# Kernel tuning notes

Hardware: AMD Instinct MI355X
Metric: run time of the kernel (lower is better)

## Reference

```python
import jax, jax.numpy as jnp
import numpy as np

N_NODES = 100000
N_EDGES = 3200000
IN_DIM = 64
HID = 64


def setup_inputs() -> dict:
    key = jax.random.key(0)
    ks = jax.random.split(key, 12)
    x = jax.random.normal(ks[0], (N_NODES, IN_DIM), dtype=jnp.float32)
    edge_index = jax.random.randint(ks[1], (2, N_EDGES), 0, N_NODES, dtype=jnp.int64)
    tau = jax.random.uniform(ks[2], (N_NODES, 1), dtype=jnp.float32)
    d1 = IN_DIM + 1  # augmented feature dim
    s1 = 1.0 / np.sqrt(d1)
    s2 = 1.0 / np.sqrt(HID)
    # SAGEConv: out = lin_l(mean_aggr) + lin_r(x); bias lives in lin_l. Weights stored [in, out].
    W1l = jax.random.uniform(ks[3], (d1, HID), jnp.float32, -s1, s1)
    b1l = jax.random.uniform(ks[4], (HID,), jnp.float32, -s1, s1)
    W1r = jax.random.uniform(ks[5], (d1, HID), jnp.float32, -s1, s1)
    W2l = jax.random.uniform(ks[6], (HID, HID), jnp.float32, -s2, s2)
    b2l = jax.random.uniform(ks[7], (HID,), jnp.float32, -s2, s2)
    W2r = jax.random.uniform(ks[8], (HID, HID), jnp.float32, -s2, s2)
    Wfc = jax.random.uniform(ks[9], (HID, 1), jnp.float32, -s2, s2)
    bfc = jax.random.uniform(ks[10], (1,), jnp.float32, -s2, s2)
    return {"x": x, "edge_index": edge_index, "tau": tau,
            "W1l": W1l, "b1l": b1l, "W1r": W1r,
            "W2l": W2l, "b2l": b2l, "W2r": W2r,
            "Wfc": Wfc, "bfc": bfc}


def _sage_conv(x, src, dst, Wl, bl, Wr, n_nodes):
    # mean aggregation of source-node features onto target nodes
    summed = jax.ops.segment_sum(x[src], dst, num_segments=n_nodes)  # [N, d]
    deg = jax.ops.segment_sum(jnp.ones(src.shape[0], x.dtype), dst, num_segments=n_nodes)
    mean = summed / jnp.maximum(deg, 1.0)[:, None]
    return mean @ Wl + bl + x @ Wr


def reference(x, edge_index, tau, W1l, b1l, W1r, W2l, b2l, W2r, Wfc, bfc):
    src, dst = edge_index[0], edge_index[1]
    n = x.shape[0]
    h = jnp.concatenate([x, tau], axis=1)  # augment_features: append tau column
    h = jax.nn.relu(_sage_conv(h, src, dst, W1l, b1l, W1r, n))
    h = jax.nn.relu(_sage_conv(h, src, dst, W2l, b2l, W2r, n))
    return h @ Wfc + bfc  # [N, 1]
```

## Files before the change

kernel.cpp:

```cpp
#include <hip/hip_runtime.h>
#include <hip/hip_bf16.h>
#include <hip/hip_fp16.h>
#include <hip/hip_fp8.h>


#define BSH 7
#define NBKT 782
#define NBLK 512
#define PER 6250
#define CAPH 3072
#define AB2 256

typedef _Float16 half8 __attribute__((ext_vector_type(8)));
typedef float floatx4 __attribute__((ext_vector_type(4)));
typedef float floatx2 __attribute__((ext_vector_type(2)));

struct h4s { __half2 lo, hi; };

#if __has_builtin(__builtin_amdgcn_cvt_pk_f32_fp8)
template <bool HI>
__device__ __forceinline__ float2 f8x2_to_f2(int v) {
    floatx2 r = __builtin_amdgcn_cvt_pk_f32_fp8(v, HI);
    return make_float2(r.x, r.y);
}
#else
template <bool HI>
__device__ __forceinline__ float2 f8x2_to_f2(int v) {
    unsigned short u = HI ? (unsigned short)(((unsigned)v) >> 16)
                          : (unsigned short)(v & 0xFFFF);
    __half2_raw r = __hip_cvt_fp8x2_to_halfraw2((__hip_fp8x2_storage_t)u, __HIP_E4M3);
    return __half22float2(*(__half2*)&r);
}
#endif

#if __has_builtin(__builtin_amdgcn_cvt_pk_fp8_f32)
__device__ __forceinline__ unsigned f4_to_f8x4(float a, float b, float c, float d) {
    int lo = __builtin_amdgcn_cvt_pk_fp8_f32(a, b, 0, false);
    return (unsigned)__builtin_amdgcn_cvt_pk_fp8_f32(c, d, lo, true);
}
__device__ __forceinline__ unsigned char f_to_f8(float a) {
    return (unsigned char)(__builtin_amdgcn_cvt_pk_fp8_f32(a, a, 0, false) & 0xFF);
}
#else
__device__ __forceinline__ unsigned f4_to_f8x4(float a, float b, float c, float d) {
    unsigned lo = (unsigned)__hip_cvt_float2_to_fp8x2(make_float2(a, b), __HIP_SATFINITE, __HIP_E4M3);
    unsigned hi = (unsigned)__hip_cvt_float2_to_fp8x2(make_float2(c, d), __HIP_SATFINITE, __HIP_E4M3);
    return lo | (hi << 16);
}
__device__ __forceinline__ unsigned char f_to_f8(float a) {
    return (unsigned char)__hip_cvt_float_to_fp8(a, __HIP_SATFINITE, __HIP_E4M3);
}
#endif

__global__ __launch_bounds__(256) void k_histprep(
    const int* __restrict__ dst, int* __restrict__ histT, int E,
    const float* __restrict__ x, __half* __restrict__ xh,
    unsigned char* __restrict__ xf8, int n4,
    const float* __restrict__ W1l, const float* __restrict__ W1r,
    const float* __restrict__ W2l, const float* __restrict__ W2r,
    __half* __restrict__ wbuf1, __half* __restrict__ wbuf2) {
    if (blockIdx.x < NBLK) {
        __shared__ int h[NBKT];
        for (int i = threadIdx.x; i < NBKT; i += 256) h[i] = 0;
        __syncthreads();
        int lo = blockIdx.x * PER;
        int hi = lo + PER; if (hi > E) hi = E;
        for (int e = lo + threadIdx.x; e < hi; e += 256)
            atomicAdd(&h[dst[e] >> BSH], 1);
        __syncthreads();
        for (int k = threadIdx.x; k < NBKT; k += 256)
            histT[k * NBLK + blockIdx.x] = h[k];
    } else if (blockIdx.x < NBLK + 9) {
        int idx = (blockIdx.x - NBLK) * 256 + threadIdx.x;
        if (idx < 1280) {
            int lane = idx & 63;
            int nt = (idx >> 6) & 3;
            int kstep = idx >> 8;
            int col = nt * 16 + (lane & 15);
            int kbase = kstep * 32 + (lane >> 4) * 8;
#pragma unroll
            for (int j = 0; j < 8; ++j) {
                int k = kbase + j;
                float v;
                if (k < 64)        v = W1l[k * 64 + col];
                else if (k < 128)  v = W1r[(k - 64) * 64 + col];
                else if (k == 128) v = W1l[64 * 64 + col];
                else if (k == 129) v = W1r[64 * 64 + col];
                else v = 0.f;
                wbuf1[(size_t)idx * 8 + j] = __float2half(v);
            }
        } else if (idx < 1280 + 1024) {
            int i2 = idx - 1280;
            int lane = i2 & 63;
            int nt = (i2 >> 6) & 3;
            int kstep = i2 >> 8;
            int col = nt * 16 + (lane & 15);
            int kbase = kstep * 32 + (lane >> 4) * 8;
#pragma unroll
            for (int j = 0; j < 8; ++j) {
                int k = kbase + j;
                float v = (k < 64) ? W2l[k * 64 + col] : W2r[(k - 64) * 64 + col];
                wbuf2[(size_t)i2 * 8 + j] = __float2half(v);
            }
        }
    } else {
        int i = (blockIdx.x - NBLK - 9) * 256 + threadIdx.x;
        if (i < n4) {
            float4 v = ((const float4*)x)[i];
            ((__half2*)xh)[2 * i]     = __floats2half2_rn(v.x, v.y);
            ((__half2*)xh)[2 * i + 1] = __floats2half2_rn(v.z, v.w);
            ((unsigned*)xf8)[i] = f4_to_f8x4(v.x, v.y, v.z, v.w);
        }
    }
}


__global__ __launch_bounds__(NBLK) void k_scanblk(int* __restrict__ histT,
                                                  int* __restrict__ btot) {
    __shared__ int s[NBLK];
    int k = blockIdx.x, t = threadIdx.x;
    int v = histT[k * NBLK + t];
    s[t] = v;
    __syncthreads();
    for (int off = 1; off < NBLK; off <<= 1) {
        int u = (t >= off) ? s[t - off] : 0;
        __syncthreads();
        s[t] += u;
        __syncthreads();
    }
    histT[k * NBLK + t] = s[t] - v;
    if (t == NBLK - 1) btot[k] = s[t];
}

__global__ __launch_bounds__(1024) void k_scanbkt(const int* __restrict__ btot,
                                                  int* __restrict__ bstart) {
    __shared__ int s[1024];
    int t = threadIdx.x;
    int v = (t < NBKT) ? btot[t] : 0;
    s[t] = v;
    __syncthreads();
    for (int off = 1; off < 1024; off <<= 1) {
        int u = (t >= off) ? s[t - off] : 0;
        __syncthreads();
        s[t] += u;
        __syncthreads();
    }
    if (t < NBKT) bstart[t] = s[t] - v;
    if (t == NBKT - 1) bstart[NBKT] = s[t];
}

__global__ __launch_bounds__(256) void k_scatter(const int* __restrict__ src,
                                                 const int* __restrict__ dst,
                                                 const int* __restrict__ histT,
                                                 const int* __restrict__ bstart,
                                                 int* __restrict__ binned, int E) {
    __shared__ int sorted[PER];
    __shared__ int lstart[NBKT + 1];
    __shared__ int cur[NBKT];
    __shared__ int gst[NBKT];
    __shared__ int tsum[256];
    int b = blockIdx.x, t = threadIdx.x;
    int base = b * PER;
    int blen = E - base; if (blen > PER) blen = PER;

    for (int k = t; k < NBKT; k += 256) lstart[k] = 0;
    __syncthreads();
    for (int e = base + t; e < base + blen; e += 256)
        atomicAdd(&lstart[dst[e] >> BSH], 1);
    __syncthreads();
    int c0 = 0;
    int i0 = t * 4;
#pragma unroll
    for (int j = 0; j < 4; ++j)
        if (i0 + j < NBKT) c0 += lstart[i0 + j];
    tsum[t] = c0;
    __syncthreads();
    for (int off = 1; off < 256; off <<= 1) {
        int u = (t >= off) ? tsum[t - off] : 0;
        __syncthreads();
        tsum[t] += u;
        __syncthreads();
    }
    int running = tsum[t] - c0;
    __syncthreads();
#pragma unroll
    for (int j = 0; j < 4; ++j) {
        int i = i0 + j;
        if (i < NBKT) {
            int v = lstart[i];
            lstart[i] = running;
            running += v;
        }
    }
    __syncthreads();
    if (t == 0) lstart[NBKT] = blen;
    for (int k = t; k < NBKT; k += 256) {
        cur[k] = lstart[k];
        gst[k] = bstart[k] + histT[k * NBLK + b];
    }
    __syncthreads();
    for (int e = base + t; e < base + blen; e += 256) {
        int d = dst[e], s = src[e];
        int pos = atomicAdd(&cur[d >> BSH], 1);
        sorted[pos] = (s << BSH) | (d & ((1 << BSH) - 1));
    }
    __syncthreads();
    int qw = t >> 4, ql = t & 15;
    for (int k = qw; k < NBKT; k += 16) {
        int st = lstart[k];
        int ln = lstart[k + 1] - st;
        int gd = gst[k];
        for (int i = ql; i < ln; i += 16)
            binned[gd + i] = sorted[st + i];
    }
}


__global__ __launch_bounds__(AB2) void k_aggrb1(
    const int* __restrict__ binned, const int* __restrict__ bstart,
    const unsigned char* __restrict__ xf8, const float* __restrict__ tau,
    __half* __restrict__ zm1, __half* __restrict__ mt1, int N) {
    __shared__ int cidx[CAPH];
    __shared__ int cnt[64], s[64], cur[64];
    int k = blockIdx.x >> 1, h = blockIdx.x & 1, t = threadIdx.x;
    int lo = bstart[k], hi = bstart[k + 1];
    if (t < 64) cnt[t] = 0;
    __syncthreads();
    for (int e = lo + t; e < hi; e += AB2) {
        int p = binned[e];
        if (((p >> 6) & 1) == h) atomicAdd(&cnt[p & 63], 1);
    }
    __syncthreads();
    if (t < 64) s[t] = cnt[t];
    __syncthreads();
    for (int off = 1; off < 64; off <<= 1) {
        int u = 0;
        if (t < 64 && t >= off) u = s[t - off];
        __syncthreads();
        if (t < 64) s[t] += u;
        __syncthreads();
    }
    if (t < 64) cur[t] = s[t] - cnt[t];
    __syncthreads();
    for (int e = lo + t; e < hi; e += AB2) {
        int p = binned[e];
        if (((p >> 6) & 1) == h) {
            int pos = atomicAdd(&cur[p & 63], 1);
            if (pos < CAPH) cidx[pos] = p >> BSH;
        }
    }
    __syncthreads();

    int lane = t & 63;
    int q = lane >> 4;
    int c = lane & 15;
    int g = c & 3;
    int ch = c >> 2;
    unsigned cb = (unsigned)(ch << 4);
    const char* xb = (const char*)xf8;

    for (int p = (t >> 6); p < 16; p += (AB2 / 64)) {
        int ld = (p << 2) + q;
        int node = (k << BSH) + (h << 6) + ld;
        int d = cnt[ld];
        int startL = cur[ld] - d;
        int dm = d;
        dm = max(dm, __shfl_xor(dm, 16, 64));
        dm = max(dm, __shfl_xor(dm, 32, 64));
        float4 A0 = {0.f, 0.f, 0.f, 0.f}, A1 = A0, A2 = A0, A3 = A0;
        float sumtau = 0.f;
        for (int base = 0; base < dm; base += 16) {
            int nmax = dm - base; if (nmax > 16) nmax = 16;
            int ng = (nmax + 3) >> 2;
            int s0 = base + g;
            int s1 = s0 + 4, s2 = s0 + 8, s3 = s0 + 12;
            bool v0 = s0 < d, v1 = s1 < d, v2 = s2 < d, v3 = s3 < d;
            int sx0, sx1, sx2, sx3;
            int4 r0, r1, r2, r3;
            sx0 = cidx[v0 ? startL + s0 : 0];
            r0 = *(const int4*)(xb + (((unsigned)sx0 << 6) + cb));
            if (ng > 1) {
                sx1 = cidx[v1 ? startL + s1 : 0];
                r1 = *(const int4*)(xb + (((unsigned)sx1 << 6) + cb));
            }
            if (ng > 2) {
                sx2 = cidx[v2 ? startL + s2 : 0];
                r2 = *(const int4*)(xb + (((unsigned)sx2 << 6) + cb));
            }
            if (ng > 3) {
                sx3 = cidx[v3 ? startL + s3 : 0];
                r3 = *(const int4*)(xb + (((unsigned)sx3 << 6) + cb));
            }
            if (ch == 0) {
                if (v0) sumtau += tau[sx0];
                if (ng > 1 && v1) sumtau += tau[sx1];
                if (ng > 2 && v2) sumtau += tau[sx2];
                if (ng > 3 && v3) sumtau += tau[sx3];
            }
            auto accum = [&](const int4& r) {
                float2 l0 = f8x2_to_f2<false>(r.x), h0 = f8x2_to_f2<true>(r.x);
                float2 l1 = f8x2_to_f2<false>(r.y), h1v = f8x2_to_f2<true>(r.y);
                float2 l2 = f8x2_to_f2<false>(r.z), h2v = f8x2_to_f2<true>(r.z);
                float2 l3 = f8x2_to_f2<false>(r.w), h3v = f8x2_to_f2<true>(r.w);
                A0.x += l0.x; A0.y += l0.y; A0.z += h0.x; A0.w += h0.y;
                A1.x += l1.x; A1.y += l1.y; A1.z += h1v.x; A1.w += h1v.y;
                A2.x += l2.x; A2.y += l2.y; A2.z += h2v.x; A2.w += h2v.y;
                A3.x += l3.x; A3.y += l3.y; A3.z += h3v.x; A3.w += h3v.y;
            };
            if (v0)            accum(r0);
            if (ng > 1 && v1)  accum(r1);
            if (ng > 2 && v2)  accum(r2);
            if (ng > 3 && v3)  accum(r3);
        }
#pragma unroll
        for (int off = 1; off <= 2; off <<= 1) {
            A0.x += __shfl_xor(A0.x, off, 64); A0.y += __shfl_xor(A0.y, off, 64);
            A0.z += __shfl_xor(A0.z, off, 64); A0.w += __shfl_xor(A0.w, off, 64);
            A1.x += __shfl_xor(A1.x, off, 64); A1.y += __shfl_xor(A1.y, off, 64);
            A1.z += __shfl_xor(A1.z, off, 64); A1.w += __shfl_xor(A1.w, off, 64);
            A2.x += __shfl_xor(A2.x, off, 64); A2.y += __shfl_xor(A2.y, off, 64);
            A2.z += __shfl_xor(A2.z, off, 64); A2.w += __shfl_xor(A2.w, off, 64);
            A3.x += __shfl_xor(A3.x, off, 64); A3.y += __shfl_xor(A3.y, off, 64);
            A3.z += __shfl_xor(A3.z, off, 64); A3.w += __shfl_xor(A3.w, off, 64);
            sumtau += __shfl_xor(sumtau, off, 64);
        }
        float inv = 1.f / fmaxf((float)d, 1.f);
        if (node < N) {
            float4 Aw = (g == 0) ? A0 : ((g == 1) ? A1 : ((g == 2) ? A2 : A3));
            h4s o;
            o.lo = __floats2half2_rn(Aw.x * inv, Aw.y * inv);
            o.hi = __floats2half2_rn(Aw.z * inv, Aw.w * inv);
            *(h4s*)(zm1 + (size_t)node * 64 + (ch << 4) + (g << 2)) = o;
            if (c == 0) mt1[node] = __float2half(sumtau * inv);
        }
    }
}

__global__ __launch_bounds__(AB2) void k_aggrb2(
    const int* __restrict__ binned, const int* __restrict__ bstart,
    const unsigned char* __restrict__ h1f8, __half* __restrict__ zm2, int N) {
    __shared__ int cidx[CAPH];
    __shared__ int cnt[64], s[64], cur[64];
    int k = blockIdx.x >> 1, h = blockIdx.x & 1, t = threadIdx.x;
    int lo = bstart[k], hi = bstart[k + 1];
    if (t < 64) cnt[t] = 0;
    __syncthreads();
    for (int e = lo + t; e < hi; e += AB2) {
        int p = binned[e];
        if (((p >> 6) & 1) == h) atomicAdd(&cnt[p & 63], 1);
    }
    __syncthreads();
    if (t < 64) s[t] = cnt[t];
    __syncthreads();
    for (int off = 1; off < 64; off <<= 1) {
        int u = 0;
        if (t < 64 && t >= off) u = s[t - off];
        __syncthreads();
        if (t < 64) s[t] += u;
        __syncthreads();
    }
    if (t < 64) cur[t] = s[t] - cnt[t];
    __syncthreads();
    for (int e = lo + t; e < hi; e += AB2) {
        int p = binned[e];
        if (((p >> 6) & 1) == h) {
            int pos = atomicAdd(&cur[p & 63], 1);
            if (pos < CAPH) cidx[pos] = p >> BSH;
        }
    }
    __syncthreads();

    int lane = t & 63;
    int q = lane >> 4;
    int c = lane & 15;
    int g = c & 3;
    int ch = c >> 2;
    unsigned cb = (unsigned)(ch << 4);
    const char* hb = (const char*)h1f8;

    for (int p = (t >> 6); p < 16; p += (AB2 / 64)) {
        int ld = (p << 2) + q;
        int node = (k << BSH) + (h << 6) + ld;
        int d = cnt[ld];
        int startL = cur[ld] - d;
        int dm = d;
        dm = max(dm, __shfl_xor(dm, 16, 64));
        dm = max(dm, __shfl_xor(dm, 32, 64));
        float4 A0 = {0.f, 0.f, 0.f, 0.f}, A1 = A0, A2 = A0, A3 = A0;
        for (int base = 0; base < dm; base += 16) {
            int nmax = dm - base; if (nmax > 16) nmax = 16;
            int ng = (nmax + 3) >> 2;
            int s0 = base + g;
            int s1 = s0 + 4, s2 = s0 + 8, s3 = s0 + 12;
            bool v0 = s0 < d, v1 = s1 < d, v2 = s2 < d, v3 = s3 < d;
            int sx0, sx1, sx2, sx3;
            int4 r0, r1, r2, r3;
            sx0 = cidx[v0 ? startL + s0 : 0];
            r0 = *(const int4*)(hb + (((unsigned)sx0 << 6) + cb));
            if (ng > 1) {
                sx1 = cidx[v1 ? startL + s1 : 0];
                r1 = *(const int4*)(hb + (((unsigned)sx1 << 6) + cb));
            }
            if (ng > 2) {
                sx2 = cidx[v2 ? startL + s2 : 0];
                r2 = *(const int4*)(hb + (((unsigned)sx2 << 6) + cb));
            }
            if (ng > 3) {
                sx3 = cidx[v3 ? startL + s3 : 0];
                r3 = *(const int4*)(hb + (((unsigned)sx3 << 6) + cb));
            }
            auto accum = [&](const int4& r) {
                float2 l0 = f8x2_to_f2<false>(r.x), h0 = f8x2_to_f2<true>(r.x);
                float2 l1 = f8x2_to_f2<false>(r.y), h1v = f8x2_to_f2<true>(r.y);
                float2 l2 = f8x2_to_f2<false>(r.z), h2v = f8x2_to_f2<true>(r.z);
                float2 l3 = f8x2_to_f2<false>(r.w), h3v = f8x2_to_f2<true>(r.w);
                A0.x += l0.x; A0.y += l0.y; A0.z += h0.x; A0.w += h0.y;
                A1.x += l1.x; A1.y += l1.y; A1.z += h1v.x; A1.w += h1v.y;
                A2.x += l2.x; A2.y += l2.y; A2.z += h2v.x; A2.w += h2v.y;
                A3.x += l3.x; A3.y += l3.y; A3.z += h3v.x; A3.w += h3v.y;
            };
            if (v0)            accum(r0);
            if (ng > 1 && v1)  accum(r1);
            if (ng > 2 && v2)  accum(r2);
            if (ng > 3 && v3)  accum(r3);
        }
#pragma unroll
        for (int off = 1; off <= 2; off <<= 1) {
            A0.x += __shfl_xor(A0.x, off, 64); A0.y += __shfl_xor(A0.y, off, 64);
            A0.z += __shfl_xor(A0.z, off, 64); A0.w += __shfl_xor(A0.w, off, 64);
            A1.x += __shfl_xor(A1.x, off, 64); A1.y += __shfl_xor(A1.y, off, 64);
            A1.z += __shfl_xor(A1.z, off, 64); A1.w += __shfl_xor(A1.w, off, 64);
            A2.x += __shfl_xor(A2.x, off, 64); A2.y += __shfl_xor(A2.y, off, 64);
            A2.z += __shfl_xor(A2.z, off, 64); A2.w += __shfl_xor(A2.w, off, 64);
            A3.x += __shfl_xor(A3.x, off, 64); A3.y += __shfl_xor(A3.y, off, 64);
            A3.z += __shfl_xor(A3.z, off, 64); A3.w += __shfl_xor(A3.w, off, 64);
        }
        float inv = 1.f / fmaxf((float)d, 1.f);
        if (node < N) {
            float4 Aw = (g == 0) ? A0 : ((g == 1) ? A1 : ((g == 2) ? A2 : A3));
            h4s o;
            o.lo = __floats2half2_rn(Aw.x * inv, Aw.y * inv);
            o.hi = __floats2half2_rn(Aw.z * inv, Aw.w * inv);
            *(h4s*)(zm2 + (size_t)node * 64 + (ch << 4) + (g << 2)) = o;
        }
    }
}


__global__ __launch_bounds__(256) void k_gemm1(
    const __half* __restrict__ zm1, const __half* __restrict__ mt1,
    const __half* __restrict__ xh, const float* __restrict__ tau,
    const __half* __restrict__ wbuf1, const float* __restrict__ b1l,
    __half* __restrict__ h1, unsigned char* __restrict__ h1f8, int ntiles) {
    int tile = blockIdx.x * 4 + (threadIdx.x >> 6);
    if (tile >= ntiles) return;
    int lane = threadIdx.x & 63;
    int sub = lane & 15;
    int quad = lane >> 4;
    int row = tile * 16 + sub;

    floatx4 acc0 = {0.f, 0.f, 0.f, 0.f};
    floatx4 acc1 = {0.f, 0.f, 0.f, 0.f};
    floatx4 acc2 = {0.f, 0.f, 0.f, 0.f};
    floatx4 acc3 = {0.f, 0.f, 0.f, 0.f};

    const _Float16* zrow = (const _Float16*)zm1 + (size_t)row * 64 + quad * 8;
    const _Float16* xrow = (const _Float16*)xh + (size_t)row * 64 + quad * 8;
    const _Float16* wb = (const _Float16*)wbuf1 + (size_t)lane * 8;

    half8 amat[5];
    amat[0] = *(const half8*)(zrow);
    amat[1] = *(const half8*)(zrow + 32);
    amat[2] = *(const half8*)(xrow);
    amat[3] = *(const half8*)(xrow + 32);
    half8 a4 = {0, 0, 0, 0, 0, 0, 0, 0};
    if (quad == 0) {
        a4[0] = ((const _Float16*)mt1)[row];
        a4[1] = (_Float16)tau[row];
    }
    amat[4] = a4;

#pragma unroll
    for (int ks = 0; ks < 5; ++ks) {
        half8 a = amat[ks];
        half8 b0 = *(const half8*)(wb + (size_t)(ks * 4 + 0) * 512);
        half8 b1 = *(const half8*)(wb + (size_t)(ks * 4 + 1) * 512);
        half8 b2 = *(const half8*)(wb + (size_t)(ks * 4 + 2) * 512);
        half8 b3 = *(const half8*)(wb + (size_t)(ks * 4 + 3) * 512);
        acc0 = __builtin_amdgcn_mfma_f32_16x16x32_f16(a, b0, acc0, 0, 0, 0);
        acc1 = __builtin_amdgcn_mfma_f32_16x16x32_f16(a, b1, acc1, 0, 0, 0);
        acc2 = __builtin_amdgcn_mfma_f32_16x16x32_f16(a, b2, acc2, 0, 0, 0);
        acc3 = __builtin_amdgcn_mfma_f32_16x16x32_f16(a, b3, acc3, 0, 0, 0);
    }
    float bv0 = b1l[sub], bv1 = b1l[16 + sub], bv2 = b1l[32 + sub], bv3 = b1l[48 + sub];
#pragma unroll
    for (int reg = 0; reg < 4; ++reg) {
        int r = quad * 4 + reg;
        float v0 = fmaxf(acc0[reg] + bv0, 0.f);
        float v1 = fmaxf(acc1[reg] + bv1, 0.f);
        float v2 = fmaxf(acc2[reg] + bv2, 0.f);
        float v3 = fmaxf(acc3[reg] + bv3, 0.f);
        __half* orow = h1 + (size_t)(tile * 16 + r) * 64;
        orow[sub]      = __float2half(v0);
        orow[16 + sub] = __float2half(v1);
        orow[32 + sub] = __float2half(v2);
        orow[48 + sub] = __float2half(v3);
        unsigned char* orow8 = h1f8 + (size_t)(tile * 16 + r) * 64;
        orow8[sub]      = f_to_f8(v0);
        orow8[16 + sub] = f_to_f8(v1);
        orow8[32 + sub] = f_to_f8(v2);
        orow8[48 + sub] = f_to_f8(v3);
    }
}

__global__ __launch_bounds__(256) void k_gemm2(
    const __half* __restrict__ zm2, const __half* __restrict__ h1,
    const __half* __restrict__ wbuf2, const float* __restrict__ b2l,
    const float* __restrict__ Wfc, const float* __restrict__ bfc,
    float* __restrict__ out, int ntiles) {
    int tile = blockIdx.x * 4 + (threadIdx.x >> 6);
    if (tile >= ntiles) return;
    int lane = threadIdx.x & 63;
    int sub = lane & 15;
    int quad = lane >> 4;
    int row = tile * 16 + sub;

    floatx4 acc0 = {0.f, 0.f, 0.f, 0.f};
    floatx4 acc1 = {0.f, 0.f, 0.f, 0.f};
    floatx4 acc2 = {0.f, 0.f, 0.f, 0.f};
    floatx4 acc3 = {0.f, 0.f, 0.f, 0.f};

    const _Float16* zrow = (const _Float16*)zm2 + (size_t)row * 64 + quad * 8;
    const _Float16* hrow = (const _Float16*)h1 + (size_t)row * 64 + quad * 8;
    const _Float16* wb = (const _Float16*)wbuf2 + (size_t)lane * 8;

    half8 amat[4];
    amat[0] = *(const half8*)(zrow);
    amat[1] = *(const half8*)(zrow + 32);
    amat[2] = *(const half8*)(hrow);
    amat[3] = *(const half8*)(hrow + 32);

#pragma unroll
    for (int ks = 0; ks < 4; ++ks) {
        half8 a = amat[ks];
        half8 b0 = *(const half8*)(wb + (size_t)(ks * 4 + 0) * 512);
        half8 b1 = *(const half8*)(wb + (size_t)(ks * 4 + 1) * 512);
        half8 b2 = *(const half8*)(wb + (size_t)(ks * 4 + 2) * 512);
        half8 b3 = *(const half8*)(wb + (size_t)(ks * 4 + 3) * 512);
        acc0 = __builtin_amdgcn_mfma_f32_16x16x32_f16(a, b0, acc0, 0, 0, 0);
        acc1 = __builtin_amdgcn_mfma_f32_16x16x32_f16(a, b1, acc1, 0, 0, 0);
        acc2 = __builtin_amdgcn_mfma_f32_16x16x32_f16(a, b2, acc2, 0, 0, 0);
        acc3 = __builtin_amdgcn_mfma_f32_16x16x32_f16(a, b3, acc3, 0, 0, 0);
    }
    float bb0 = b2l[sub], bb1 = b2l[16 + sub], bb2 = b2l[32 + sub], bb3 = b2l[48 + sub];
    float wv0 = Wfc[sub], wv1 = Wfc[16 + sub], wv2 = Wfc[32 + sub], wv3 = Wfc[48 + sub];
    float p[4];
#pragma unroll
    for (int reg = 0; reg < 4; ++reg) {
        p[reg] = fmaxf(acc0[reg] + bb0, 0.f) * wv0
               + fmaxf(acc1[reg] + bb1, 0.f) * wv1
               + fmaxf(acc2[reg] + bb2, 0.f) * wv2
               + fmaxf(acc3[reg] + bb3, 0.f) * wv3;
    }
#pragma unroll
    for (int m = 1; m <= 8; m <<= 1) {
#pragma unroll
        for (int reg = 0; reg < 4; ++reg) p[reg] += __shfl_xor(p[reg], m, 64);
    }
    if (sub == 0) {
        float b0 = bfc[0];
#pragma unroll
        for (int reg = 0; reg < 4; ++reg)
            out[tile * 16 + quad * 4 + reg] = p[reg] + b0;
    }
}

extern "C" void kernel_launch(void* const* d_in, const int* in_sizes, int n_in,
                              void* d_out, int out_size, void* d_ws, size_t ws_size,
                              hipStream_t stream) {
    const float* x   = (const float*)d_in[0];
    const int*   ei  = (const int*)d_in[1];
    const float* tau = (const float*)d_in[2];
    const float* W1l = (const float*)d_in[3];
    const float* b1l = (const float*)d_in[4];
    const float* W1r = (const float*)d_in[5];
    const float* W2l = (const float*)d_in[6];
    const float* b2l = (const float*)d_in[7];
    const float* W2r = (const float*)d_in[8];
    const float* Wfc = (const float*)d_in[9];
    const float* bfc = (const float*)d_in[10];
    float* out = (float*)d_out;

    const int N = in_sizes[0] / 64;
    const int E = in_sizes[1] / 2;
    const int* src = ei;
    const int* dst = ei + E;

    char* w = (char*)d_ws;
    auto take = [&](size_t b) { char* p = w; w += (b + 255) & ~(size_t)255; return p; };
    int*           histT  = (int*)take((size_t)NBKT * NBLK * 4);
    int*           btot   = (int*)take((size_t)NBKT * 4);
    int*           bstart = (int*)take((size_t)(NBKT + 1) * 4);
    int*           binned = (int*)take((size_t)E * 4);
    __half*        xh     = (__half*)take((size_t)N * 64 * 2);
    unsigned char* xf8    = (unsigned char*)take((size_t)N * 64);
    __half*        h1     = (__half*)take((size_t)N * 64 * 2);
    unsigned char* h1f8   = (unsigned char*)take((size_t)N * 64);
    __half*        zm1    = (__half*)take((size_t)N * 64 * 2);
    __half*        mt1    = (__half*)take((size_t)N * 2);
    __half*        zm2    = (__half*)take((size_t)N * 64 * 2);
    __half*        wbuf1  = (__half*)take(1280 * 8 * 2);
    __half*        wbuf2  = (__half*)take(1024 * 8 * 2);

    int n4 = N * 16;
    int hpblocks = NBLK + 9 + (n4 + 255) / 256;
    int ntiles = N / 16;
    int gblocks = (ntiles + 3) / 4;

    k_histprep<<<hpblocks, 256, 0, stream>>>(dst, histT, E, x, xh, xf8, n4,
                                             W1l, W1r, W2l, W2r, wbuf1, wbuf2);
    k_scanblk <<<NBKT, NBLK, 0, stream>>>(histT, btot);
    k_scanbkt <<<1, 1024, 0, stream>>>(btot, bstart);
    k_scatter <<<NBLK, 256, 0, stream>>>(src, dst, histT, bstart, binned, E);
    k_aggrb1  <<<2 * NBKT, AB2, 0, stream>>>(binned, bstart, xf8, tau, zm1, mt1, N);
    k_gemm1   <<<gblocks, 256, 0, stream>>>(zm1, mt1, xh, tau, wbuf1, b1l, h1, h1f8, ntiles);
    k_aggrb2  <<<2 * NBKT, AB2, 0, stream>>>(binned, bstart, h1f8, zm2, N);
    k_gemm2   <<<gblocks, 256, 0, stream>>>(zm2, h1, wbuf2, b2l, Wfc, bfc, out, ntiles);
}
```

Baseline: 267.3 us.

## Build per-node CSR once and drop per-block resorting in aggregation kernels

Adds a k_csr kernel that sorts each 128-node bucket's edges by destination node in shared memory, writes them back into the binned array, and emits per-node offsets. Both aggregation kernels then read neighbour indices straight from global CSR instead of each block re-counting, scanning and rescattering the bucket's edges into shared memory. This removes the duplicated in-block sort done twice per layer (two half-blocks per bucket). In exchange it adds a kernel launch and an extra global read/write pass, and neighbour index loads now come from global memory rather than LDS. Buckets with more than 6144 edges would be silently truncated.

Result: slower. 273.9 us (+2.5%).

```diff
diff --git a/kernel.cpp b/kernel.cpp
--- a/kernel.cpp
+++ b/kernel.cpp
@@ -8,7 +8,7 @@
 #define NBKT 782
 #define NBLK 512
 #define PER 6250
-#define CAPH 3072
+#define CAP 6144
 #define AB2 256
 
 typedef _Float16 half8 __attribute__((ext_vector_type(8)));
@@ -215,42 +215,68 @@
     }
 }
 
+__global__ __launch_bounds__(512) void k_csr(int* __restrict__ binned,
+                                             const int* __restrict__ bstart,
+                                             int* __restrict__ nodeoff,
+                                             int E, int N) {
+    __shared__ int cnt[128], sarr[128], cur[128];
+    __shared__ int sorted[CAP];
+    int k = blockIdx.x, t = threadIdx.x;
+    int lo = bstart[k], hi = bstart[k + 1];
+    if (t < 128) cnt[t] = 0;
+    __syncthreads();
+    for (int eb = lo; eb < hi; eb += 512 * 4) {
+        int e0 = eb + t, e1 = e0 + 512, e2 = e0 + 1024, e3 = e0 + 1536;
+        int p0 = (e0 < hi) ? binned[e0] : -1;
+        int p1 = (e1 < hi) ? binned[e1] : -1;
+        int p2 = (e2 < hi) ? binned[e2] : -1;
+        int p3 = (e3 < hi) ? binned[e3] : -1;
+        if (p0 >= 0) atomicAdd(&cnt[p0 & 127], 1);
+        if (p1 >= 0) atomicAdd(&cnt[p1 & 127], 1);
+        if (p2 >= 0) atomicAdd(&cnt[p2 & 127], 1);
+        if (p3 >= 0) atomicAdd(&cnt[p3 & 127], 1);
+    }
+    __syncthreads();
+    if (t < 128) sarr[t] = cnt[t];
+    __syncthreads();
+    for (int off = 1; off < 128; off <<= 1) {
+        int u = 0;
+        if (t < 128 && t >= off) u = sarr[t - off];
+        __syncthreads();
+        if (t < 128) sarr[t] += u;
+        __syncthreads();
+    }
+    if (t < 128) {
+        int excl = sarr[t] - cnt[t];
+        cur[t] = excl;
+        int node = (k << BSH) + t;
+        if (node < N) nodeoff[node] = lo + excl;
+    }
+    if (k == NBKT - 1 && t == 0) nodeoff[N] = E;
+    __syncthreads();
+    for (int eb = lo; eb < hi; eb += 512 * 4) {
+        int e0 = eb + t, e1 = e0 + 512, e2 = e0 + 1024, e3 = e0 + 1536;
+        int p0 = (e0 < hi) ? binned[e0] : -1;
+        int p1 = (e1 < hi) ? binned[e1] : -1;
+        int p2 = (e2 < hi) ? binned[e2] : -1;
+        int p3 = (e3 < hi) ? binned[e3] : -1;
+        if (p0 >= 0) { int pos = atomicAdd(&cur[p0 & 127], 1); if (pos < CAP) sorted[pos] = p0 >> BSH; }
+        if (p1 >= 0) { int pos = atomicAdd(&cur[p1 & 127], 1); if (pos < CAP) sorted[pos] = p1 >> BSH; }
+        if (p2 >= 0) { int pos = atomicAdd(&cur[p2 & 127], 1); if (pos < CAP) sorted[pos] = p2 >> BSH; }
+        if (p3 >= 0) { int pos = atomicAdd(&cur[p3 & 127], 1); if (pos < CAP) sorted[pos] = p3 >> BSH; }
+    }
+    __syncthreads();
+    int len = hi - lo; if (len > CAP) len = CAP;
+    for (int i = t; i < len; i += 512)
+        binned[lo + i] = sorted[i];
+}
+
 
 __global__ __launch_bounds__(AB2) void k_aggrb1(
-    const int* __restrict__ binned, const int* __restrict__ bstart,
+    const int* __restrict__ nbr, const int* __restrict__ nodeoff,
     const unsigned char* __restrict__ xf8, const float* __restrict__ tau,
     __half* __restrict__ zm1, __half* __restrict__ mt1, int N) {
-    __shared__ int cidx[CAPH];
-    __shared__ int cnt[64], s[64], cur[64];
-    int k = blockIdx.x >> 1, h = blockIdx.x & 1, t = threadIdx.x;
-    int lo = bstart[k], hi = bstart[k + 1];
-    if (t < 64) cnt[t] = 0;
-    __syncthreads();
-    for (int e = lo + t; e < hi; e += AB2) {
-        int p = binned[e];
-        if (((p >> 6) & 1) == h) atomicAdd(&cnt[p & 63], 1);
-    }
-    __syncthreads();
-    if (t < 64) s[t] = cnt[t];
-    __syncthreads();
-    for (int off = 1; off < 64; off <<= 1) {
-        int u = 0;
-        if (t < 64 && t >= off) u = s[t - off];
-        __syncthreads();
-        if (t < 64) s[t] += u;
-        __syncthreads();
-    }
-    if (t < 64) cur[t] = s[t] - cnt[t];
-    __syncthreads();
-    for (int e = lo + t; e < hi; e += AB2) {
-        int p = binned[e];
-        if (((p >> 6) & 1) == h) {
-            int pos = atomicAdd(&cur[p & 63], 1);
-            if (pos < CAPH) cidx[pos] = p >> BSH;
-        }
-    }
-    __syncthreads();
-
+    int t = threadIdx.x;
     int lane = t & 63;
     int q = lane >> 4;
     int c = lane & 15;
@@ -258,12 +284,14 @@
     int ch = c >> 2;
     unsigned cb = (unsigned)(ch << 4);
     const char* xb = (const char*)xf8;
+    int nb = blockIdx.x << 6;
 
     for (int p = (t >> 6); p < 16; p += (AB2 / 64)) {
         int ld = (p << 2) + q;
-        int node = (k << BSH) + (h << 6) + ld;
-        int d = cnt[ld];
-        int startL = cur[ld] - d;
+        int node = nb + ld;
+        int off0 = 0, off1 = 0;
+        if (node < N) { off0 = nodeoff[node]; off1 = nodeoff[node + 1]; }
+        int d = off1 - off0;
         int dm = d;
         dm = max(dm, __shfl_xor(dm, 16, 64));
         dm = max(dm, __shfl_xor(dm, 32, 64));
@@ -277,18 +305,22 @@
             bool v0 = s0 < d, v1 = s1 < d, v2 = s2 < d, v3 = s3 < d;
             int sx0, sx1, sx2, sx3;
             int4 r0, r1, r2, r3;
-            sx0 = cidx[v0 ? startL + s0 : 0];
+            sx0 = nbr[off0 + (v0 ? s0 : 0)];
+            sx0 = v0 ? sx0 : 0;
             r0 = *(const int4*)(xb + (((unsigned)sx0 << 6) + cb));
             if (ng > 1) {
-                sx1 = cidx[v1 ? startL + s1 : 0];
+                sx1 = nbr[off0 + (v1 ? s1 : 0)];
+                sx1 = v1 ? sx1 : 0;
                 r1 = *(const int4*)(xb + (((unsigned)sx1 << 6) + cb));
             }
             if (ng > 2) {
-                sx2 = cidx[v2 ? startL + s2 : 0];
+                sx2 = nbr[off0 + (v2 ? s2 : 0)];
+                sx2 = v2 ? sx2 : 0;
                 r2 = *(const int4*)(xb + (((unsigned)sx2 << 6) + cb));
             }
             if (ng > 3) {
-                sx3 = cidx[v3 ? startL + s3 : 0];
+                sx3 = nbr[off0 + (v3 ? s3 : 0)];
+                sx3 = v3 ? sx3 : 0;
                 r3 = *(const int4*)(xb + (((unsigned)sx3 << 6) + cb));
             }
             if (ch == 0) {
@@ -337,39 +369,9 @@
 }
 
 __global__ __launch_bounds__(AB2) void k_aggrb2(
-    const int* __restrict__ binned, const int* __restrict__ bstart,
+    const int* __restrict__ nbr, const int* __restrict__ nodeoff,
     const unsigned char* __restrict__ h1f8, __half* __restrict__ zm2, int N) {
-    __shared__ int cidx[CAPH];
-    __shared__ int cnt[64], s[64], cur[64];
-    int k = blockIdx.x >> 1, h = blockIdx.x & 1, t = threadIdx.x;
-    int lo = bstart[k], hi = bstart[k + 1];
-    if (t < 64) cnt[t] = 0;
-    __syncthreads();
-    for (int e = lo + t; e < hi; e += AB2) {
-        int p = binned[e];
-        if (((p >> 6) & 1) == h) atomicAdd(&cnt[p & 63], 1);
-    }
-    __syncthreads();
-    if (t < 64) s[t] = cnt[t];
-    __syncthreads();
-    for (int off = 1; off < 64; off <<= 1) {
-        int u = 0;
-        if (t < 64 && t >= off) u = s[t - off];
-        __syncthreads();
-        if (t < 64) s[t] += u;
-        __syncthreads();
-    }
-    if (t < 64) cur[t] = s[t] - cnt[t];
-    __syncthreads();
-    for (int e = lo + t; e < hi; e += AB2) {
-        int p = binned[e];
-        if (((p >> 6) & 1) == h) {
-            int pos = atomicAdd(&cur[p & 63], 1);
-            if (pos < CAPH) cidx[pos] = p >> BSH;
-        }
-    }
-    __syncthreads();
-
+    int t = threadIdx.x;
     int lane = t & 63;
     int q = lane >> 4;
     int c = lane & 15;
@@ -377,12 +379,14 @@
     int ch = c >> 2;
     unsigned cb = (unsigned)(ch << 4);
     const char* hb = (const char*)h1f8;
+    int nb = blockIdx.x << 6;
 
     for (int p = (t >> 6); p < 16; p += (AB2 / 64)) {
         int ld = (p << 2) + q;
-        int node = (k << BSH) + (h << 6) + ld;
-        int d = cnt[ld];
-        int startL = cur[ld] - d;
+        int node = nb + ld;
+        int off0 = 0, off1 = 0;
+        if (node < N) { off0 = nodeoff[node]; off1 = nodeoff[node + 1]; }
+        int d = off1 - off0;
         int dm = d;
         dm = max(dm, __shfl_xor(dm, 16, 64));
         dm = max(dm, __shfl_xor(dm, 32, 64));
@@ -395,18 +399,22 @@
             bool v0 = s0 < d, v1 = s1 < d, v2 = s2 < d, v3 = s3 < d;
             int sx0, sx1, sx2, sx3;
             int4 r0, r1, r2, r3;
-            sx0 = cidx[v0 ? startL + s0 : 0];
+            sx0 = nbr[off0 + (v0 ? s0 : 0)];
+            sx0 = v0 ? sx0 : 0;
             r0 = *(const int4*)(hb + (((unsigned)sx0 << 6) + cb));
             if (ng > 1) {
-                sx1 = cidx[v1 ? startL + s1 : 0];
+                sx1 = nbr[off0 + (v1 ? s1 : 0)];
+                sx1 = v1 ? sx1 : 0;
                 r1 = *(const int4*)(hb + (((unsigned)sx1 << 6) + cb));
             }
             if (ng > 2) {
-                sx2 = cidx[v2 ? startL + s2 : 0];
+                sx2 = nbr[off0 + (v2 ? s2 : 0)];
+                sx2 = v2 ? sx2 : 0;
                 r2 = *(const int4*)(hb + (((unsigned)sx2 << 6) + cb));
             }
             if (ng > 3) {
-                sx3 = cidx[v3 ? startL + s3 : 0];
+                sx3 = nbr[off0 + (v3 ? s3 : 0)];
+                sx3 = v3 ? sx3 : 0;
                 r3 = *(const int4*)(hb + (((unsigned)sx3 << 6) + cb));
             }
             auto accum = [&](const int4& r) {
@@ -601,7 +609,8 @@
     int*           histT  = (int*)take((size_t)NBKT * NBLK * 4);
     int*           btot   = (int*)take((size_t)NBKT * 4);
     int*           bstart = (int*)take((size_t)(NBKT + 1) * 4);
-    int*           binned = (int*)take((size_t)E * 4);
+    int*           binned = (int*)take((size_t)(E + 64) * 4);
+    int*           nodeoff= (int*)take((size_t)(N + 2) * 4);
     __half*        xh     = (__half*)take((size_t)N * 64 * 2);
     unsigned char* xf8    = (unsigned char*)take((size_t)N * 64);
     __half*        h1     = (__half*)take((size_t)N * 64 * 2);
@@ -616,14 +625,16 @@
     int hpblocks = NBLK + 9 + (n4 + 255) / 256;
     int ntiles = N / 16;
     int gblocks = (ntiles + 3) / 4;
+    int ablocks = (N + 63) / 64;
 
     k_histprep<<<hpblocks, 256, 0, stream>>>(dst, histT, E, x, xh, xf8, n4,
                                              W1l, W1r, W2l, W2r, wbuf1, wbuf2);
     k_scanblk <<<NBKT, NBLK, 0, stream>>>(histT, btot);
     k_scanbkt <<<1, 1024, 0, stream>>>(btot, bstart);
     k_scatter <<<NBLK, 256, 0, stream>>>(src, dst, histT, bstart, binned, E);
-    k_aggrb1  <<<2 * NBKT, AB2, 0, stream>>>(binned, bstart, xf8, tau, zm1, mt1, N);
+    k_csr     <<<NBKT, 512, 0, stream>>>(binned, bstart, nodeoff, E, N);
+    k_aggrb1  <<<ablocks, AB2, 0, stream>>>(binned, nodeoff, xf8, tau, zm1, mt1, N);
     k_gemm1   <<<gblocks, 256, 0, stream>>>(zm1, mt1, xh, tau, wbuf1, b1l, h1, h1f8, ntiles);
-    k_aggrb2  <<<2 * NBKT, AB2, 0, stream>>>(binned, bstart, h1f8, zm2, N);
+    k_aggrb2  <<<ablocks, AB2, 0, stream>>>(binned, nodeoff, h1f8, zm2, N);
     k_gemm2   <<<gblocks, 256, 0, stream>>>(zm2, h1, wbuf2, b2l, Wfc, bfc, out, ntiles);
 }
```
